# Optimization experiments

Hardware: AMD Instinct MI355X
Metric: run time of the kernel (lower is better)

## Reference

```python
import jax, jax.numpy as jnp
import numpy as np

B, S, DM, L = 128, 168, 128, 2
I, N, R, K, P = 256, 16, 8, 4, 24


def setup_inputs() -> dict:
    key = jax.random.key(0)
    ks = iter(jax.random.split(key, 32))
    rn = lambda shape, s=0.02: jax.random.normal(next(ks), shape, jnp.float32) * s
    return {
        'x_load': jax.random.normal(next(ks), (B, S, 1), jnp.float32),
        'x_img': jax.random.normal(next(ks), (B, S, 64), jnp.float32),
        'x_text': jax.random.normal(next(ks), (B, S, 768), jnp.float32),
        'Wl': rn((DM, 1)), 'Wi': rn((DM, 64)), 'Wt': rn((DM, 768)),
        'b_fuse': jnp.zeros((DM,), jnp.float32),
        'mnorm_w': jnp.ones((L, DM), jnp.float32),
        'in_w': rn((L, 2 * I, DM)), 'in_b': jnp.zeros((L, 2 * I), jnp.float32),
        'conv_w': rn((L, I, K), 0.3), 'conv_b': jnp.zeros((L, I), jnp.float32),
        'xp_w': rn((L, R + 2 * N, I)),
        'dt_w': rn((L, I, R), 0.1), 'dt_b': rn((L, I), 0.1),
        'A_log': rn((L, I, N), 1.0),
        'Dp': jnp.ones((L, I), jnp.float32),
        'out_w': rn((L, DM, I)), 'out_b': jnp.zeros((L, DM), jnp.float32),
        'fnorm_w': jnp.ones((DM,), jnp.float32),
        'ln_w': jnp.ones((DM,), jnp.float32), 'ln_b': jnp.zeros((DM,), jnp.float32),
        'fc_w': rn((P, DM)), 'fc_b': jnp.zeros((P,), jnp.float32),
    }


def rmsnorm(x, w, eps=1e-5):
    return x * jax.lax.rsqrt(jnp.mean(x * x, -1, keepdims=True) + eps) * w


def layernorm(x, w, b, eps=1e-5):
    m = jnp.mean(x, -1, keepdims=True)
    v = jnp.mean((x - m) ** 2, -1, keepdims=True)
    return (x - m) * jax.lax.rsqrt(v + eps) * w + b


def ssm_scan(dA, dBu, C):
    # dA, dBu: [B,S,I,N]; C: [B,S,N] -> y: [B,S,I]
    def step(state, inp):
        dA_s, dBu_s, C_s = inp
        state = dA_s * state + dBu_s                      # [B,I,N]
        y = jnp.einsum('bin,bn->bi', state, C_s)
        return state, y
    init = jnp.zeros_like(dA[:, 0])
    xs = (dA.transpose(1, 0, 2, 3), dBu.transpose(1, 0, 2, 3), C.transpose(1, 0, 2))
    _, ys = jax.lax.scan(step, init, xs)
    return ys.transpose(1, 0, 2)


def mamba_mixer(h, in_w, in_b, conv_w, conv_b, xp_w, dt_w, dt_b, A_log, Dp, out_w, out_b):
    hs_gate = h @ in_w.T + in_b                           # [B,S,2I]
    hs, gate = jnp.split(hs_gate, 2, axis=-1)
    u = hs.transpose(0, 2, 1)                             # [B,I,S]
    pad = jnp.pad(u, ((0, 0), (0, 0), (K - 1, 0)))        # causal depthwise conv
    u = sum(conv_w[None, :, k, None] * pad[:, :, k:k + S] for k in range(K))
    u = jax.nn.silu(u + conv_b[None, :, None])
    ut = u.transpose(0, 2, 1)                             # [B,S,I]
    sp = ut @ xp_w.T                                      # [B,S,R+2N]
    dt_in, Bm, Cm = jnp.split(sp, [R, R + N], axis=-1)
    dt = jax.nn.softplus(dt_in @ dt_w.T + dt_b)           # [B,S,I]
    A = -jnp.exp(A_log)                                   # [I,N]
    dA = jnp.exp(dt[..., None] * A[None, None])           # [B,S,I,N]
    dBu = dt[..., None] * Bm[:, :, None, :] * ut[..., None]
    y = ssm_scan(dA, dBu, Cm)                             # [B,S,I]
    y = y + ut * Dp[None, None, :]
    y = y * jax.nn.silu(gate)
    return y @ out_w.T + out_b


def reference(x_load, x_img, x_text, Wl, Wi, Wt, b_fuse, mnorm_w, in_w, in_b,
              conv_w, conv_b, xp_w, dt_w, dt_b, A_log, Dp, out_w, out_b,
              fnorm_w, ln_w, ln_b, fc_w, fc_b):
    # shared feature fusion -> [B,S,DM]
    h = x_load @ Wl.T + x_img @ Wi.T + x_text @ Wt.T + b_fuse
    for l in range(L):
        h = h + mamba_mixer(rmsnorm(h, mnorm_w[l]), in_w[l], in_b[l], conv_w[l],
                            conv_b[l], xp_w[l], dt_w[l], dt_b[l], A_log[l],
                            Dp[l], out_w[l], out_b[l])
    h = rmsnorm(h, fnorm_w)
    last = layernorm(h[:, -1, :], ln_w, ln_b)
    out = last @ fc_w.T + fc_b                            # [B,P]
    return out[..., None]
```

## Files before the change

### kernel.cpp

```cpp
#include <hip/hip_runtime.h>
#include <hip/hip_bf16.h>

#define BB   128
#define SS   168
#define DM   128
#define LL   2
#define II   256
#define NN   16
#define RR   8
#define KK   4
#define PP   24
#define MROWS (BB*SS)
#define NCH  12
#define TCH  14

#define XPF  24
#define INF  128
#define OUTF 64
#define FR_TOT (LL*(XPF+INF+OUTF))

typedef __attribute__((ext_vector_type(8))) short bf16x8;
typedef __attribute__((ext_vector_type(4))) short bf16x4;
typedef __attribute__((ext_vector_type(4))) float f32x4;

__device__ __forceinline__ float wave_sum(float x) {
#pragma unroll
    for (int off = 32; off > 0; off >>= 1) x += __shfl_xor(x, off);
    return x;
}
__device__ __forceinline__ float siluf(float x) {
    return x / (1.f + __expf(-x));
}
__device__ __forceinline__ float softplusf(float x) {
    return (x > 20.f) ? x : __logf(1.f + __expf(x));
}
__device__ __forceinline__ short f2bf(float x) {
    unsigned u = __builtin_bit_cast(unsigned, x);
    u = (u + 0x7FFFu + ((u >> 16) & 1u)) >> 16;
    return (short)u;
}
__device__ __forceinline__ bf16x4 pack4(const float* f) {
    bf16x4 r;
#pragma unroll
    for (int j = 0; j < 4; ++j) r[j] = f2bf(f[j]);
    return r;
}
__device__ __forceinline__ bf16x8 pack8(const float* f) {
    bf16x8 r;
#pragma unroll
    for (int j = 0; j < 8; ++j) r[j] = f2bf(f[j]);
    return r;
}
__device__ __forceinline__ bf16x8 cvt8v(float4 a, float4 b) {
    unsigned u0, u1, u2, u3;
    asm("v_cvt_pk_bf16_f32 %0, %1, %2" : "=v"(u0) : "v"(a.x), "v"(a.y));
    asm("v_cvt_pk_bf16_f32 %0, %1, %2" : "=v"(u1) : "v"(a.z), "v"(a.w));
    asm("v_cvt_pk_bf16_f32 %0, %1, %2" : "=v"(u2) : "v"(b.x), "v"(b.y));
    asm("v_cvt_pk_bf16_f32 %0, %1, %2" : "=v"(u3) : "v"(b.z), "v"(b.w));
    union { unsigned u[4]; bf16x8 v; } r;
    r.u[0] = u0; r.u[1] = u1; r.u[2] = u2; r.u[3] = u3;
    return r.v;
}

__global__ __launch_bounds__(256)
void hn_kernel(const float* __restrict__ h, const float* __restrict__ mnw,
               short* __restrict__ hn)
{
    const int row  = blockIdx.x * 4 + (threadIdx.x >> 6);
    const int lane = threadIdx.x & 63;
    const float2 v = *(const float2*)&h[(size_t)row * DM + lane * 2];
    const float ss = wave_sum(v.x * v.x + v.y * v.y);
    const float rsv = rsqrtf(ss * (1.f / DM) + 1e-5f);
    const float2 w = *(const float2*)&mnw[lane * 2];
    short2 o;
    o.x = f2bf(v.x * rsv * w.x);
    o.y = f2bf(v.y * rsv * w.y);
    *(short2*)&hn[(size_t)row * DM + lane * 2] = o;
}

__global__ __launch_bounds__(256)
void cvtw_kernel(const float* __restrict__ xw, const float* __restrict__ inw,
                 const float* __restrict__ outw, short* __restrict__ dst)
{
    const int tid = blockIdx.x * 256 + threadIdx.x;
    if (tid >= FR_TOT * 64) return;
    const int lane = tid & 63;
    const int fg = tid >> 6;
    float4 v0 = {0.f, 0.f, 0.f, 0.f}, v1 = {0.f, 0.f, 0.f, 0.f};
    if (fg < LL * XPF) {
        const int l = fg / XPF, f = fg % XPF;
        const int nt = f >> 3, kt = f & 7;
        const int row = nt * 16 + (lane & 15);
        const int kc = kt * 32 + (lane >> 4) * 8;
        if (row < 40) {
            const float* s = xw + ((size_t)l * 40 + row) * II + kc;
            v0 = *(const float4*)s;
            v1 = *(const float4*)(s + 4);
        }
    } else if (fg < LL * (XPF + INF)) {
        const int g = fg - LL * XPF;
        const int l = g / INF, fi = g % INF;
        const int nt = fi >> 2, kt = fi & 3;
        const int row = nt * 16 + (lane & 15);
        const int kc = kt * 32 + (lane >> 4) * 8;
        const float* s = inw + ((size_t)l * 2 * II + row) * DM + kc;
        v0 = *(const float4*)s;
        v1 = *(const float4*)(s + 4);
    } else {
        const int g = fg - LL * (XPF + INF);
        const int l = g / OUTF, fo = g % OUTF;
        const int nt = fo >> 3, kt = fo & 7;
        const int row = nt * 16 + (lane & 15);
        const int kc = kt * 32 + (lane >> 4) * 8;
        const float* s = outw + ((size_t)l * DM + row) * II + kc;
        v0 = *(const float4*)s;
        v1 = *(const float4*)(s + 4);
    }
    *(bf16x8*)(dst + ((size_t)tid) * 8) = cvt8v(v0, v1);
}

#define LDT 40
template<bool ACCUM>
__global__ __launch_bounds__(256)
void gemm_mfma(const float* __restrict__ A, const short* __restrict__ Abf,
               const float* __restrict__ W, int K,
               const float* __restrict__ A2, const float* __restrict__ W2, int K2,
               const float* __restrict__ bias,
               const float* __restrict__ r1x, const float* __restrict__ r1w,
               float* __restrict__ C, int ldc)
{
    __shared__ __align__(16) short Asl[32 * LDT];
    __shared__ __align__(16) short Bsl[64 * LDT];
    const int bm = blockIdx.x * 32;
    const int bn = blockIdx.y * 64;
    const int t  = threadIdx.x;
    const int lane = t & 63;
    const int wave = t >> 6;
    const int wr = wave >> 1, wc = wave & 1;
    const int lrow = lane & 15;
    const int lk   = (lane >> 4) * 8;

    f32x4 acc[2];
    acc[0] = (f32x4){0.f, 0.f, 0.f, 0.f};
    acc[1] = (f32x4){0.f, 0.f, 0.f, 0.f};

    const int arow = t >> 3, ak = (t & 7) * 4;
    const int brow = t >> 2, bk = (t & 3) * 8;

    float av[4], bv[8];
    bf16x4 avb;

#pragma unroll 1
    for (int pass = 0; pass < 2; ++pass) {
        const bool useBf = (pass == 0) && (Abf != nullptr);
        const float* Ap = pass ? A2 : A;
        if (!Ap && !useBf) continue;
        const float* Wp = pass ? W2 : W;
        const int    Kp = pass ? K2 : K;
        const short* abptr = useBf ? Abf + (size_t)(bm + arow) * Kp + ak : nullptr;
        const float* aptr  = useBf ? nullptr : Ap + (size_t)(bm + arow) * Kp + ak;
        const float* bptr = Wp + (size_t)(bn + brow) * Kp + bk;

        if (useBf) avb = *(const bf16x4*)(abptr);
        else       *(float4*)&av[0] = *(const float4*)(aptr);
        *(float4*)&bv[0] = *(const float4*)(bptr);
        *(float4*)&bv[4] = *(const float4*)(bptr + 4);

#pragma unroll 1
        for (int k0 = 0; k0 < Kp; k0 += 32) {
            __syncthreads();
            if (useBf) *(bf16x4*)&Asl[arow * LDT + ak] = avb;
            else       *(bf16x4*)&Asl[arow * LDT + ak] = pack4(av);
            *(bf16x8*)&Bsl[brow * LDT + bk] = pack8(bv);
            __syncthreads();
            const int kn = k0 + 32;
            if (kn < Kp) {
                if (useBf) avb = *(const bf16x4*)(abptr + kn);
                else       *(float4*)&av[0] = *(const float4*)(aptr + kn);
                *(float4*)&bv[0] = *(const float4*)(bptr + kn);
                *(float4*)&bv[4] = *(const float4*)(bptr + kn + 4);
            }
            const bf16x8 af = *(const bf16x8*)&Asl[(wr * 16 + lrow) * LDT + lk];
            bf16x8 bfr[2];
#pragma unroll
            for (int ni = 0; ni < 2; ++ni)
                bfr[ni] = *(const bf16x8*)&Bsl[(wc * 32 + ni * 16 + lrow) * LDT + lk];
#pragma unroll
            for (int ni = 0; ni < 2; ++ni)
                acc[ni] = __builtin_amdgcn_mfma_f32_16x16x32_bf16(af, bfr[ni], acc[ni], 0, 0, 0);
        }
    }

#pragma unroll
    for (int r = 0; r < 4; ++r) {
        const int row = bm + wr * 16 + (lane >> 4) * 4 + r;
        const float xl = r1x ? r1x[row] : 0.f;
#pragma unroll
        for (int ni = 0; ni < 2; ++ni) {
            const int col = bn + wc * 32 + ni * 16 + lrow;
            float v = acc[ni][r];
            if (bias) v += bias[col];
            if (r1x)  v += xl * r1w[col];
            float* cp = &C[(size_t)row * ldc + col];
            if (ACCUM) v += *cp;
            *cp = v;
        }
    }
}

__global__ __launch_bounds__(256)
void fusedA_kernel(const short* __restrict__ hn, const float* __restrict__ cw,
                   const float* __restrict__ cb, const short* __restrict__ inws,
                   const short* __restrict__ xws, const float* __restrict__ inb,
                   const float* __restrict__ dtw, const float* __restrict__ dtb,
                   const float* __restrict__ A_log,
                   float* __restrict__ ut, float* __restrict__ sp,
                   float* __restrict__ dtsum_g, float* __restrict__ q)
{
    __shared__ float hsl[17][II + 4];
    __shared__ float uts[TCH][II + 4];
    __shared__ float lsp[TCH * 40];
    const int b = blockIdx.x;
    const int ch = blockIdx.y;
    const int i = threadIdx.x;
    const int s0 = ch * TCH;
    const int lane = i & 63;
    const int wv = i >> 6;
    const int lrow = lane & 15;
    const int lkg = (lane >> 4) * 8;
    const int r0 = (lane >> 4) * 4;

    {
        const short* hnb = hn + (size_t)b * SS * DM;
#pragma unroll
        for (int mt = 0; mt < 2; ++mt) {
            const int ma = mt * 16 + lrow;
            const int rga = s0 - 3 + ma;
            const bool va = (ma < 17) && (rga >= 0);
            bf16x8 af[4];
#pragma unroll
            for (int kt = 0; kt < 4; ++kt) {
                if (va) af[kt] = *(const bf16x8*)(hnb + (size_t)rga * DM + kt * 32 + lkg);
                else { bf16x8 z = {0,0,0,0,0,0,0,0}; af[kt] = z; }
            }
#pragma unroll
            for (int j = 0; j < 4; ++j) {
                const int nt = wv * 4 + j;
                f32x4 acc = (f32x4){0.f, 0.f, 0.f, 0.f};
#pragma unroll
                for (int kt = 0; kt < 4; ++kt) {
                    const bf16x8 bf = *(const bf16x8*)(inws + ((size_t)(nt * 4 + kt) * 64 + lane) * 8);
                    acc = __builtin_amdgcn_mfma_f32_16x16x32_bf16(af[kt], bf, acc, 0, 0, 0);
                }
                const int n = nt * 16 + lrow;
                const float bn_ = inb[n];
#pragma unroll
                for (int r = 0; r < 4; ++r) {
                    const int mrow = mt * 16 + r0 + r;
                    if (mrow < 17) {
                        const int rg = s0 - 3 + mrow;
                        hsl[mrow][n] = (rg < 0) ? 0.f : acc[r] + bn_;
                    }
                }
            }
        }
    }
    __syncthreads();

    {
        const float4 w = *(const float4*)&cw[i * 4];
        const float bi = cb[i];
        float* up = ut + (size_t)b * SS * II + i;
        float wm3 = hsl[0][i], wm2 = hsl[1][i], wm1 = hsl[2][i];
        for (int s = 0; s < TCH; ++s) {
            const float cur = hsl[s + 3][i];
            float a = fmaf(w.x, wm3, fmaf(w.y, wm2, fmaf(w.z, wm1, fmaf(w.w, cur, bi))));
            const float uv = siluf(a);
            up[(s0 + s) * II] = uv;
            uts[s][i] = uv;
            wm3 = wm2; wm2 = wm1; wm1 = cur;
        }
    }
    __syncthreads();

    {
        if (wv < 3) {
            const int srow = lrow;
            const short* wp = xws + ((size_t)(wv * 8) * 64 + lane) * 8;
            f32x4 acc = (f32x4){0.f, 0.f, 0.f, 0.f};
#pragma unroll
            for (int kt = 0; kt < 8; ++kt) {
                const float* up = &uts[0][0] + srow * (II + 4) + kt * 32 + lkg;
                const float4 a0 = *(const float4*)(up);
                const float4 a1 = *(const float4*)(up + 4);
                const bf16x8 af = cvt8v(a0, a1);
                const bf16x8 bf = *(const bf16x8*)(wp + (size_t)kt * 512);
                acc = __builtin_amdgcn_mfma_f32_16x16x32_bf16(af, bf, acc, 0, 0, 0);
            }
            const int col = wv * 16 + lrow;
            if (col < 40) {
#pragma unroll
                for (int r = 0; r < 4; ++r)
                    if (r0 + r < TCH) lsp[(r0 + r) * 40 + col] = acc[r];
            }
        }
    }
    __syncthreads();

    {
        float* spp = sp + ((size_t)b * SS + s0) * 40;
        for (int idx = i; idx < TCH * 40; idx += 256) spp[idx] = lsp[idx];
    }

    float dw[8];
    {
        const float4 w0 = *(const float4*)&dtw[i * 8];
        const float4 w1 = *(const float4*)&dtw[i * 8 + 4];
        dw[0]=w0.x; dw[1]=w0.y; dw[2]=w0.z; dw[3]=w0.w;
        dw[4]=w1.x; dw[5]=w1.y; dw[6]=w1.z; dw[7]=w1.w;
    }
    const float bdt = dtb[i];
    float Ar[NN];
#pragma unroll
    for (int n = 0; n < NN; ++n) Ar[n] = -__expf(A_log[i * NN + n]);

    float st[NN];
#pragma unroll
    for (int n = 0; n < NN; ++n) st[n] = 0.f;
    float dtsum = 0.f;

    for (int s = 0; s < TCH; ++s) {
        const float uv = uts[s][i];
        const float* r = &lsp[s * 40];
        const float p0 = fmaf(r[1], dw[1], r[0] * dw[0]);
        const float p1 = fmaf(r[3], dw[3], r[2] * dw[2]);
        const float p2 = fmaf(r[5], dw[5], r[4] * dw[4]);
        const float p3 = fmaf(r[7], dw[7], r[6] * dw[6]);
        const float dtv = softplusf(bdt + (p0 + p1) + (p2 + p3));
        const float du = dtv * uv;
        dtsum += dtv;
#pragma unroll
        for (int n = 0; n < NN; ++n) {
            const float a = __expf(dtv * Ar[n]);
            st[n] = fmaf(a, st[n], du * r[8 + n]);
        }
    }
    dtsum_g[((size_t)b * NCH + ch) * II + i] = dtsum;
    float* qp = q + (((size_t)b * NCH + ch) * NN) * II + i;
#pragma unroll
    for (int n = 0; n < NN; ++n) qp[n * II] = st[n];
}

__global__ __launch_bounds__(256)
void combine_kernel(const float* __restrict__ dtsum_g,
                    const float* __restrict__ A_log, float* __restrict__ q)
{
    const int b = blockIdx.x;
    const int i = threadIdx.x;
    float Ar[NN];
#pragma unroll
    for (int n = 0; n < NN; ++n) Ar[n] = -__expf(A_log[i * NN + n]);
    float ds[NCH];
#pragma unroll
    for (int ch = 0; ch < NCH; ++ch)
        ds[ch] = dtsum_g[((size_t)b * NCH + ch) * II + i];
#pragma unroll
    for (int n = 0; n < NN; ++n) {
        float cur = 0.f;
#pragma unroll
        for (int ch = 0; ch < NCH; ++ch) {
            const size_t idx = (((size_t)b * NCH + ch) * NN + n) * II + i;
            const float Pv = __expf(Ar[n] * ds[ch]);
            const float qv = q[idx];
            q[idx] = cur;
            cur = fmaf(Pv, cur, qv);
        }
    }
}

#define YLD 296
__global__ __launch_bounds__(256)
void scanB_kernel(const float* __restrict__ ut, const float* __restrict__ sp,
                  const float* __restrict__ qinit, const short* __restrict__ inws,
                  const short* __restrict__ outws, const short* __restrict__ hn,
                  const float* __restrict__ inb, const float* __restrict__ outb,
                  const float* __restrict__ dtw, const float* __restrict__ dtb,
                  const float* __restrict__ A_log, const float* __restrict__ Dp,
                  float* __restrict__ h)
{
    __shared__ float gsl[TCH][II + 4];
    __shared__ float lsp[TCH * 40];
    __shared__ __align__(16) short ygl[16 * YLD];
    const int b = blockIdx.x;
    const int ch = blockIdx.y;
    const int i = threadIdx.x;
    const int s0 = ch * TCH;
    const int lane = i & 63;
    const int wv = i >> 6;
    const int lrow = lane & 15;
    const int lkg = (lane >> 4) * 8;
    const int r0 = (lane >> 4) * 4;

    ygl[14 * YLD + i] = 0; ygl[15 * YLD + i] = 0;

    {
        const short* hnb = hn + (size_t)b * SS * DM;
        const bool va = (lrow < TCH);
        const int rga = s0 + lrow;
        bf16x8 af[4];
#pragma unroll
        for (int kt = 0; kt < 4; ++kt) {
            if (va) af[kt] = *(const bf16x8*)(hnb + (size_t)rga * DM + kt * 32 + lkg);
            else { bf16x8 z = {0,0,0,0,0,0,0,0}; af[kt] = z; }
        }
#pragma unroll
        for (int j = 0; j < 4; ++j) {
            const int nt = 16 + wv * 4 + j;
            f32x4 acc = (f32x4){0.f, 0.f, 0.f, 0.f};
#pragma unroll
            for (int kt = 0; kt < 4; ++kt) {
                const bf16x8 bf = *(const bf16x8*)(inws + ((size_t)(nt * 4 + kt) * 64 + lane) * 8);
                acc = __builtin_amdgcn_mfma_f32_16x16x32_bf16(af[kt], bf, acc, 0, 0, 0);
            }
            const int n = (nt - 16) * 16 + lrow;
            const float bn_ = inb[256 + n];
#pragma unroll
            for (int r = 0; r < 4; ++r)
                if (r0 + r < TCH) gsl[r0 + r][n] = acc[r] + bn_;
        }
    }

    {
        const float* spp = sp + ((size_t)b * SS + s0) * 40;
        for (int idx = i; idx < TCH * 40; idx += 256) lsp[idx] = spp[idx];
    }
    float dw[8];
    {
        const float4 w0 = *(const float4*)&dtw[i * 8];
        const float4 w1 = *(const float4*)&dtw[i * 8 + 4];
        dw[0]=w0.x; dw[1]=w0.y; dw[2]=w0.z; dw[3]=w0.w;
        dw[4]=w1.x; dw[5]=w1.y; dw[6]=w1.z; dw[7]=w1.w;
    }
    const float bdt = dtb[i];
    const float Dv = Dp[i];
    float Ar[NN];
#pragma unroll
    for (int n = 0; n < NN; ++n) Ar[n] = -__expf(A_log[i * NN + n]);

    float st[NN];
    {
        const float* qp = qinit + (((size_t)b * NCH + ch) * NN) * II + i;
#pragma unroll
        for (int n = 0; n < NN; ++n) st[n] = qp[n * II];
    }

    const float* utp = ut + ((size_t)b * SS + s0) * II + i;
    __syncthreads();

    float uv = utp[0];
    for (int s = 0; s < TCH; ++s) {
        const int sn = (s + 1 < TCH) ? s + 1 : s;
        const float uv_n = utp[sn * II];
        const float* r = &lsp[s * 40];
        const float p0 = fmaf(r[1], dw[1], r[0] * dw[0]);
        const float p1 = fmaf(r[3], dw[3], r[2] * dw[2]);
        const float p2 = fmaf(r[5], dw[5], r[4] * dw[4]);
        const float p3 = fmaf(r[7], dw[7], r[6] * dw[6]);
        const float dtv = softplusf(bdt + (p0 + p1) + (p2 + p3));
        const float du = dtv * uv;
        float y0 = 0.f, y1 = 0.f, y2 = 0.f, y3 = 0.f;
#pragma unroll
        for (int n = 0; n < NN; n += 4) {
            const float a0 = __expf(dtv * Ar[n + 0]);
            const float a1 = __expf(dtv * Ar[n + 1]);
            const float a2 = __expf(dtv * Ar[n + 2]);
            const float a3 = __expf(dtv * Ar[n + 3]);
            st[n + 0] = fmaf(a0, st[n + 0], du * r[8 + n + 0]);
            st[n + 1] = fmaf(a1, st[n + 1], du * r[8 + n + 1]);
            st[n + 2] = fmaf(a2, st[n + 2], du * r[8 + n + 2]);
            st[n + 3] = fmaf(a3, st[n + 3], du * r[8 + n + 3]);
            y0 = fmaf(st[n + 0], r[24 + n + 0], y0);
            y1 = fmaf(st[n + 1], r[24 + n + 1], y1);
            y2 = fmaf(st[n + 2], r[24 + n + 2], y2);
            y3 = fmaf(st[n + 3], r[24 + n + 3], y3);
        }
        const float yv = (y0 + y1) + (y2 + y3) + uv * Dv;
        ygl[s * YLD + i] = f2bf(yv * siluf(gsl[s][i]));
        uv = uv_n;
    }
    __syncthreads();

    {
        bf16x8 af[8];
#pragma unroll
        for (int kt = 0; kt < 8; ++kt)
            af[kt] = *(const bf16x8*)&ygl[lrow * YLD + kt * 32 + lkg];
#pragma unroll
        for (int j = 0; j < 2; ++j) {
            const int nt = wv * 2 + j;
            f32x4 acc = (f32x4){0.f, 0.f, 0.f, 0.f};
#pragma unroll
            for (int kt = 0; kt < 8; ++kt) {
                const bf16x8 bf = *(const bf16x8*)(outws + ((size_t)(nt * 8 + kt) * 64 + lane) * 8);
                acc = __builtin_amdgcn_mfma_f32_16x16x32_bf16(af[kt], bf, acc, 0, 0, 0);
            }
            const int col = nt * 16 + lrow;
            const float bo = outb[col];
#pragma unroll
            for (int r = 0; r < 4; ++r) {
                const int srow = r0 + r;
                if (srow < TCH) {
                    float* hp = &h[((size_t)b * SS + s0 + srow) * DM + col];
                    *hp += acc[r] + bo;
                }
            }
        }
    }
}

__global__ __launch_bounds__(64)
void final_kernel(const float* __restrict__ h, const float* __restrict__ fnw,
                  const float* __restrict__ lnw, const float* __restrict__ lnb,
                  const float* __restrict__ fcw, const float* __restrict__ fcb,
                  float* __restrict__ out)
{
    __shared__ float last[DM];
    const int b = blockIdx.x;
    const int lane = threadIdx.x;
    const float* hp = &h[((size_t)b * SS + (SS - 1)) * DM];
    const float2 v = *(const float2*)&hp[lane * 2];
    const float ss = wave_sum(v.x * v.x + v.y * v.y);
    const float sc = rsqrtf(ss * (1.f / DM) + 1e-5f);
    const float2 fw = *(const float2*)&fnw[lane * 2];
    const float t0 = v.x * sc * fw.x, t1 = v.y * sc * fw.y;
    const float m = wave_sum(t0 + t1) * (1.f / DM);
    const float d0 = t0 - m, d1 = t1 - m;
    const float var = wave_sum(d0 * d0 + d1 * d1) * (1.f / DM);
    const float iv = rsqrtf(var + 1e-5f);
    const float2 lw = *(const float2*)&lnw[lane * 2];
    const float2 lb = *(const float2*)&lnb[lane * 2];
    last[lane * 2]     = d0 * iv * lw.x + lb.x;
    last[lane * 2 + 1] = d1 * iv * lw.y + lb.y;
    __syncthreads();
    if (lane < PP) {
        float a = fcb[lane];
#pragma unroll 8
        for (int d = 0; d < DM; ++d) a = fmaf(last[d], fcw[lane * DM + d], a);
        out[b * PP + lane] = a;
    }
}

extern "C" void kernel_launch(void* const* d_in, const int* in_sizes, int n_in,
                              void* d_out, int out_size, void* d_ws, size_t ws_size,
                              hipStream_t stream)
{
    (void)in_sizes; (void)n_in; (void)out_size; (void)ws_size;
    const float* x_load = (const float*)d_in[0];
    const float* x_img  = (const float*)d_in[1];
    const float* x_text = (const float*)d_in[2];
    const float* Wl     = (const float*)d_in[3];
    const float* Wi     = (const float*)d_in[4];
    const float* Wt     = (const float*)d_in[5];
    const float* b_fuse = (const float*)d_in[6];
    const float* mnorm_w= (const float*)d_in[7];
    const float* in_w   = (const float*)d_in[8];
    const float* in_b   = (const float*)d_in[9];
    const float* conv_w = (const float*)d_in[10];
    const float* conv_b = (const float*)d_in[11];
    const float* xp_w   = (const float*)d_in[12];
    const float* dt_w   = (const float*)d_in[13];
    const float* dt_b   = (const float*)d_in[14];
    const float* A_log  = (const float*)d_in[15];
    const float* Dp     = (const float*)d_in[16];
    const float* out_w  = (const float*)d_in[17];
    const float* out_b  = (const float*)d_in[18];
    const float* fnorm_w= (const float*)d_in[19];
    const float* ln_w   = (const float*)d_in[20];
    const float* ln_b   = (const float*)d_in[21];
    const float* fc_w   = (const float*)d_in[22];
    const float* fc_b   = (const float*)d_in[23];

    float* ws  = (float*)d_ws;
    float* h     = ws;
    float* ut    = h  + (size_t)MROWS * DM;
    float* sp    = ut + (size_t)MROWS * II;
    float* q     = sp + (size_t)MROWS * 40;
    float* dtsum = q  + (size_t)BB * NCH * NN * II;
    short* pool  = (short*)(dtsum + (size_t)BB * NCH * II);
    short* hn    = pool + (size_t)FR_TOT * 512;

    cvtw_kernel<<<(FR_TOT * 64 + 255) / 256, 256, 0, stream>>>(
        xp_w, in_w, out_w, pool);

    gemm_mfma<false><<<dim3(MROWS / 32, 2), 256, 0, stream>>>(
        x_text, nullptr, Wt, 768, x_img, Wi, 64, b_fuse, x_load, Wl,
        h, DM);

    for (int l = 0; l < LL; ++l) {
        const short* xws   = pool + (size_t)l * XPF * 512;
        const short* inws  = pool + (size_t)(LL * XPF + l * INF) * 512;
        const short* outws = pool + (size_t)(LL * (XPF + INF) + l * OUTF) * 512;
        hn_kernel<<<MROWS / 4, 256, 0, stream>>>(h, mnorm_w + l * DM, hn);
        fusedA_kernel<<<dim3(BB, NCH), 256, 0, stream>>>(
            hn, conv_w + l * II * KK, conv_b + l * II, inws, xws,
            in_b + (size_t)l * 2 * II,
            dt_w + l * II * RR, dt_b + l * II, A_log + l * II * NN,
            ut, sp, dtsum, q);
        combine_kernel<<<BB, 256, 0, stream>>>(dtsum, A_log + l * II * NN, q);
        scanB_kernel<<<dim3(BB, NCH), 256, 0, stream>>>(
            ut, sp, q, inws, outws, hn,
            in_b + (size_t)l * 2 * II, out_b + l * DM,
            dt_w + l * II * RR, dt_b + l * II,
            A_log + l * II * NN, Dp + l * II, h);
    }

    final_kernel<<<BB, 64, 0, stream>>>(h, fnorm_w, ln_w, ln_b, fc_w, fc_b,
                                        (float*)d_out);
}
```

Before: 201.8 us.

## Recompute in-projection and conv in scan kernel instead of storing ut

Removes the global ut buffer. fusedA no longer writes the conv+SiLU output, and scanB recomputes the in-projection (hs half) and depthwise conv on the fly from hn into shared memory. This trades a global write and read of a B*S*I float tensor per layer for extra MFMA work and about 17 KB more shared memory per block in scanB. The extra LDS could lower occupancy.

Result: slower. 216.7 us (+7.4%).

```diff
diff --git a/kernel.cpp b/kernel.cpp
--- a/kernel.cpp
+++ b/kernel.cpp
@@ -214,7 +214,7 @@
                    const short* __restrict__ xws, const float* __restrict__ inb,
                    const float* __restrict__ dtw, const float* __restrict__ dtb,
                    const float* __restrict__ A_log,
-                   float* __restrict__ ut, float* __restrict__ sp,
+                   float* __restrict__ sp,
                    float* __restrict__ dtsum_g, float* __restrict__ q)
 {
     __shared__ float hsl[17][II + 4];
@@ -270,14 +270,11 @@
     {
         const float4 w = *(const float4*)&cw[i * 4];
         const float bi = cb[i];
-        float* up = ut + (size_t)b * SS * II + i;
         float wm3 = hsl[0][i], wm2 = hsl[1][i], wm1 = hsl[2][i];
         for (int s = 0; s < TCH; ++s) {
             const float cur = hsl[s + 3][i];
             float a = fmaf(w.x, wm3, fmaf(w.y, wm2, fmaf(w.z, wm1, fmaf(w.w, cur, bi))));
-            const float uv = siluf(a);
-            up[(s0 + s) * II] = uv;
-            uts[s][i] = uv;
+            uts[s][i] = siluf(a);
             wm3 = wm2; wm2 = wm1; wm1 = cur;
         }
     }
@@ -380,14 +377,16 @@
 
 #define YLD 296
 __global__ __launch_bounds__(256)
-void scanB_kernel(const float* __restrict__ ut, const float* __restrict__ sp,
-                  const float* __restrict__ qinit, const short* __restrict__ inws,
-                  const short* __restrict__ outws, const short* __restrict__ hn,
+void scanB_kernel(const float* __restrict__ sp, const float* __restrict__ qinit,
+                  const short* __restrict__ inws, const short* __restrict__ outws,
+                  const short* __restrict__ hn,
                   const float* __restrict__ inb, const float* __restrict__ outb,
+                  const float* __restrict__ cw, const float* __restrict__ cb,
                   const float* __restrict__ dtw, const float* __restrict__ dtb,
                   const float* __restrict__ A_log, const float* __restrict__ Dp,
                   float* __restrict__ h)
 {
+    __shared__ float hsl[17][II + 4];
     __shared__ float gsl[TCH][II + 4];
     __shared__ float lsp[TCH * 40];
     __shared__ __align__(16) short ygl[16 * YLD];
@@ -403,8 +402,44 @@
 
     ygl[14 * YLD + i] = 0; ygl[15 * YLD + i] = 0;
 
-    {
-        const short* hnb = hn + (size_t)b * SS * DM;
+    const short* hnb = hn + (size_t)b * SS * DM;
+
+    {
+#pragma unroll
+        for (int mt = 0; mt < 2; ++mt) {
+            const int ma = mt * 16 + lrow;
+            const int rga = s0 - 3 + ma;
+            const bool va = (ma < 17) && (rga >= 0);
+            bf16x8 af[4];
+#pragma unroll
+            for (int kt = 0; kt < 4; ++kt) {
+                if (va) af[kt] = *(const bf16x8*)(hnb + (size_t)rga * DM + kt * 32 + lkg);
+                else { bf16x8 z = {0,0,0,0,0,0,0,0}; af[kt] = z; }
+            }
+#pragma unroll
+            for (int j = 0; j < 4; ++j) {
+                const int nt = wv * 4 + j;
+                f32x4 acc = (f32x4){0.f, 0.f, 0.f, 0.f};
+#pragma unroll
+                for (int kt = 0; kt < 4; ++kt) {
+                    const bf16x8 bf = *(const bf16x8*)(inws + ((size_t)(nt * 4 + kt) * 64 + lane) * 8);
+                    acc = __builtin_amdgcn_mfma_f32_16x16x32_bf16(af[kt], bf, acc, 0, 0, 0);
+                }
+                const int n = nt * 16 + lrow;
+                const float bn_ = inb[n];
+#pragma unroll
+                for (int r = 0; r < 4; ++r) {
+                    const int mrow = mt * 16 + r0 + r;
+                    if (mrow < 17) {
+                        const int rg = s0 - 3 + mrow;
+                        hsl[mrow][n] = (rg < 0) ? 0.f : acc[r] + bn_;
+                    }
+                }
+            }
+        }
+    }
+
+    {
         const bool va = (lrow < TCH);
         const int rga = s0 + lrow;
         bf16x8 af[4];
@@ -434,6 +469,20 @@
         const float* spp = sp + ((size_t)b * SS + s0) * 40;
         for (int idx = i; idx < TCH * 40; idx += 256) lsp[idx] = spp[idx];
     }
+    __syncthreads();
+
+    {
+        const float4 w = *(const float4*)&cw[i * 4];
+        const float bi = cb[i];
+        float wm3 = hsl[0][i], wm2 = hsl[1][i], wm1 = hsl[2][i];
+        for (int s = 0; s < TCH; ++s) {
+            const float cur = hsl[s + 3][i];
+            float a = fmaf(w.x, wm3, fmaf(w.y, wm2, fmaf(w.z, wm1, fmaf(w.w, cur, bi))));
+            hsl[s][i] = siluf(a);
+            wm3 = wm2; wm2 = wm1; wm1 = cur;
+        }
+    }
+
     float dw[8];
     {
         const float4 w0 = *(const float4*)&dtw[i * 8];
@@ -454,13 +503,8 @@
         for (int n = 0; n < NN; ++n) st[n] = qp[n * II];
     }
 
-    const float* utp = ut + ((size_t)b * SS + s0) * II + i;
-    __syncthreads();
-
-    float uv = utp[0];
     for (int s = 0; s < TCH; ++s) {
-        const int sn = (s + 1 < TCH) ? s + 1 : s;
-        const float uv_n = utp[sn * II];
+        const float uv = hsl[s][i];
         const float* r = &lsp[s * 40];
         const float p0 = fmaf(r[1], dw[1], r[0] * dw[0]);
         const float p1 = fmaf(r[3], dw[3], r[2] * dw[2]);
@@ -486,7 +530,6 @@
         }
         const float yv = (y0 + y1) + (y2 + y3) + uv * Dv;
         ygl[s * YLD + i] = f2bf(yv * siluf(gsl[s][i]));
-        uv = uv_n;
     }
     __syncthreads();
 
@@ -582,8 +625,7 @@
 
     float* ws  = (float*)d_ws;
     float* h     = ws;
-    float* ut    = h  + (size_t)MROWS * DM;
-    float* sp    = ut + (size_t)MROWS * II;
+    float* sp    = h  + (size_t)MROWS * DM;
     float* q     = sp + (size_t)MROWS * 40;
     float* dtsum = q  + (size_t)BB * NCH * NN * II;
     short* pool  = (short*)(dtsum + (size_t)BB * NCH * II);
@@ -605,11 +647,12 @@
             hn, conv_w + l * II * KK, conv_b + l * II, inws, xws,
             in_b + (size_t)l * 2 * II,
             dt_w + l * II * RR, dt_b + l * II, A_log + l * II * NN,
-            ut, sp, dtsum, q);
+            sp, dtsum, q);
         combine_kernel<<<BB, 256, 0, stream>>>(dtsum, A_log + l * II * NN, q);
         scanB_kernel<<<dim3(BB, NCH), 256, 0, stream>>>(
-            ut, sp, q, inws, outws, hn,
+            sp, q, inws, outws, hn,
             in_b + (size_t)l * 2 * II, out_b + l * DM,
+            conv_w + l * II * KK, conv_b + l * II,
             dt_w + l * II * RR, dt_b + l * II,
             A_log + l * II * NN, Dp + l * II, h);
     }
```
